# Kernel optimization log

Hardware: AMD Instinct MI355X
Metric: run time of the kernel (lower is better)

The kernel has to match this reference:

```python
import jax, jax.numpy as jnp
import numpy as np

NX, NY, NZ = 128, 128, 8
N_VOX = NX * NY * NZ
V, C, HF, WF = 6, 64, 116, 200
PAD_H, PAD_W = 928.0, 1600.0  # img_pad_shape (input image after padding)
IMG_H, IMG_W = 928.0, 1600.0  # img_shape used for the valid-flag bounds check


def _make_proj_mats():
    # Structured lidar2img matrices: pinhole intrinsics + 6 yaw-distributed cameras.
    K = np.array([[500.0, 0, 400, 0], [0, 500.0, 232, 0], [0, 0, 1, 0], [0, 0, 0, 1]], dtype=np.float64)
    A = np.array([[0.0, -1, 0], [0, 0, -1], [1, 0, 0]], dtype=np.float64)  # lidar(x fwd,y left,z up)->cam(z fwd)
    mats = []
    for j in range(V):
        yaw = 2.0 * np.pi * j / V
        c, s = np.cos(yaw), np.sin(yaw)
        Rz = np.array([[c, s, 0], [-s, c, 0], [0, 0, 1]])
        T = np.eye(4)
        T[:3, :3] = A @ Rz
        T[:3, 3] = np.array([0.0, -1.0, 0.0])
        mats.append(K @ T)
    return jnp.asarray(np.stack(mats), dtype=jnp.float32)


def setup_inputs() -> dict:
    key = jax.random.key(0)
    k1, k2 = jax.random.split(key)
    x_fov = jax.random.normal(k1, (1, V, C, HF, WF), dtype=jnp.float32)
    lo = jnp.array([-50.0, -50.0, -5.0], jnp.float32)
    span = jnp.array([100.0, 100.0, 8.0], jnp.float32)
    points = jax.random.uniform(k2, (N_VOX, 3), dtype=jnp.float32) * span + lo
    proj_mats = _make_proj_mats()
    return {"x_fov": x_fov, "points": points, "proj_mats": proj_mats}


def _bilinear_sample(feat, px, py):
    # feat [C,HF,WF]; px/py [N] in feature-map pixel coords.
    # Matches F.grid_sample(mode='bilinear', padding_mode='zeros', align_corners=False).
    x0 = jnp.floor(px)
    y0 = jnp.floor(py)
    wx1 = px - x0
    wy1 = py - y0

    def gather(xi, yi, w):
        inb = (xi >= 0) & (xi < WF) & (yi >= 0) & (yi < HF)
        xc = jnp.clip(xi, 0, WF - 1).astype(jnp.int32)
        yc = jnp.clip(yi, 0, HF - 1).astype(jnp.int32)
        return feat[:, yc, xc] * (w * inb)[None, :]  # [C,N]

    return (gather(x0, y0, (1 - wx1) * (1 - wy1))
            + gather(x0 + 1, y0, wx1 * (1 - wy1))
            + gather(x0, y0 + 1, (1 - wx1) * wy1)
            + gather(x0 + 1, y0 + 1, wx1 * wy1))


def _forward(x_fov, points, proj_mats):
    n = points.shape[0]
    # points_cam2img: homogeneous projection, perspective divide
    pts_h = jnp.concatenate([points, jnp.ones((n, 1), points.dtype)], axis=-1)  # [N,4]
    cam = jnp.einsum('vij,nj->vni', proj_mats, pts_h)  # [V,N,4]
    depth = cam[..., 2]
    d_safe = jnp.where(jnp.abs(depth) > 1e-6, depth, 1e-6)
    u = cam[..., 0] / d_safe  # image-plane x in input-image pixels (scale=1, crop=0, no flip)
    v = cam[..., 1] / d_safe
    # valid_flag: in front of camera and inside img_shape
    valid = (depth > 0) & (u > 0) & (u < IMG_W) & (v > 0) & (v < IMG_H)  # [V,N]
    # normalize by img_pad_shape then map to feature-map pixels (align_corners=False)
    px = u / PAD_W * WF - 0.5
    py = v / PAD_H * HF - 0.5
    feats = jax.vmap(_bilinear_sample)(x_fov[0], px, py)  # [V,C,N]
    feats = feats * valid[:, None, :].astype(feats.dtype)
    vol = feats.sum(0)  # [C,N] masked sum over views
    cnt = valid.sum(0).astype(feats.dtype)  # [N]
    vol = jnp.where(cnt > 0, vol, 0.0) / jnp.clip(cnt, 0.001)[None, :]
    # reshape(n_voxels[::-1] + [-1]).permute(3,2,1,0) -> [C,NX,NY,NZ]
    out = jnp.transpose(vol.reshape(C, NZ, NY, NX), (0, 3, 2, 1))
    return out[None]  # [1,C,NX,NY,NZ]


def reference(x_fov, points, proj_mats):
    return _forward(x_fov, points, proj_mats)
```

## Files before the change

### kernel.cpp

```cpp
#include <hip/hip_runtime.h>
#include <hip/hip_bf16.h>
#include <hip/hip_fp16.h>

#define NXv 128
#define NYv 128
#define NZv 8
#define NVOX (NXv * NYv * NZv)
#define NV 6
#define NC 64
#define HFv 116
#define WFv 200
#define PLANE (HFv * WFv)

#define FT_BYTES ((size_t)NV * PLANE * NC * 2)

__device__ inline unsigned int f2bf(float f) {
  unsigned int x = __float_as_uint(f);
  unsigned int r = x + 0x7fffu + ((x >> 16) & 1u);
  return (r >> 16) & 0xffffu;
}
__device__ inline float bf_lo(unsigned int q) { return __uint_as_float(q << 16); }
__device__ inline float bf_hi(unsigned int q) { return __uint_as_float(q & 0xffff0000u); }

__device__ inline unsigned short f2h_bits(float f) {
  __half h = __float2half(f);
  return *reinterpret_cast<unsigned short*>(&h);
}
__device__ inline float h_bits2f(unsigned short u) {
  __half_raw r; r.x = u;
  __half h = *reinterpret_cast<__half*>(&r);
  return __half2float(h);
}

__global__ __launch_bounds__(256) void transpose_feat_bf16(
    const float* __restrict__ in, unsigned int* __restrict__ out32) {
  __shared__ float tile[64][65];
  const int v  = blockIdx.y;
  const int p0 = blockIdx.x * 64;
  const float* src = in + (size_t)v * NC * PLANE;
  unsigned int* dst = out32 + (size_t)v * PLANE * (NC / 2);
  const int t = threadIdx.x;

#pragma unroll
  for (int i = 0; i < 4; ++i) {
    const int idx = i * 256 + t;
    const int c  = idx >> 4;
    const int p4 = idx & 15;
    const int pp = p0 + p4 * 4;
    if (pp < PLANE) {
      const float4 f = *(const float4*)(src + (size_t)c * PLANE + pp);
      tile[p4 * 4 + 0][c] = f.x;
      tile[p4 * 4 + 1][c] = f.y;
      tile[p4 * 4 + 2][c] = f.z;
      tile[p4 * 4 + 3][c] = f.w;
    }
  }
  __syncthreads();

#pragma unroll
  for (int i = 0; i < 2; ++i) {
    const int idx = i * 256 + t;
    const int p   = idx >> 3;
    const int c8  = idx & 7;
    const int pp  = p0 + p;
    if (pp < PLANE) {
      uint4 w;
      w.x = f2bf(tile[p][c8 * 8 + 0]) | (f2bf(tile[p][c8 * 8 + 1]) << 16);
      w.y = f2bf(tile[p][c8 * 8 + 2]) | (f2bf(tile[p][c8 * 8 + 3]) << 16);
      w.z = f2bf(tile[p][c8 * 8 + 4]) | (f2bf(tile[p][c8 * 8 + 5]) << 16);
      w.w = f2bf(tile[p][c8 * 8 + 6]) | (f2bf(tile[p][c8 * 8 + 7]) << 16);
      *(uint4*)(dst + (size_t)pp * 32 + c8 * 4) = w;
    }
  }
}

__global__ __launch_bounds__(256, 8) void gather_fused(
    const uint4* __restrict__ feat4,
    const float* __restrict__ points,
    const float* __restrict__ proj,
    float* __restrict__ out) {
  __shared__ unsigned short tile_h[64][66];
  __shared__ uint4 pdl[64 * NV];
  __shared__ int   cntl[64];
  __shared__ float invl[64];
  __shared__ float projl[96];

  const int bi   = blockIdx.x;
  const int xcd  = bi & 7;
  const int r    = bi >> 3;
  const int tid  = xcd * 2 + (r >> 7);
  const int q    = r & 127;
  const int ix   = (tid & 3) * 32 + (q & 31);
  const int iyg  = (tid >> 2) * 4 + (q >> 5);
  const int iy0g = iyg * 8;

  const int t    = threadIdx.x;
  const int lane = t & 63;
  const int wave = t >> 6;

  if (t < 96) projl[t] = proj[t];
  if (t < 64) cntl[t] = 0;
  __syncthreads();

  for (int task = t; task < 64 * NV; task += 256) {
    const int slot = task / NV;
    const int v    = task - slot * NV;
    const int j    = slot >> 3;
    const int iz   = slot & 7;
    const int n    = iz * (NXv * NYv) + (iy0g + j) * NXv + ix;

    const float x = points[n * 3 + 0];
    const float y = points[n * 3 + 1];
    const float z = points[n * 3 + 2];

    const float* M = projl + v * 16;
    const float cx = M[0] * x + M[1] * y + M[2]  * z + M[3];
    const float cy = M[4] * x + M[5] * y + M[6]  * z + M[7];
    const float cz = M[8] * x + M[9] * y + M[10] * z + M[11];

    const float dz = (fabsf(cz) > 1e-6f) ? cz : 1e-6f;
    const float u  = cx / dz;
    const float vv = cy / dz;

    const bool valid = (cz > 0.0f) && (u > 0.0f) && (u < 1600.0f) &&
                       (vv > 0.0f) && (vv < 928.0f);
    if (valid) {
      const float px = u  / 1600.0f * 200.0f - 0.5f;
      const float py = vv / 928.0f  * 116.0f - 0.5f;
      const float fx0 = floorf(px);
      const float fy0 = floorf(py);
      const float wx1 = px - fx0;
      const float wy1 = py - fy0;
      const float wx0 = 1.0f - wx1;
      const float wy0 = 1.0f - wy1;
      const int ix0 = (int)fx0;
      const int iy0 = (int)fy0;

      const bool bx0 = (ix0 >= 0) && (ix0 < WFv);
      const bool bx1 = (ix0 + 1 >= 0) && (ix0 + 1 < WFv);
      const bool by0 = (iy0 >= 0) && (iy0 < HFv);
      const bool by1 = (iy0 + 1 >= 0) && (iy0 + 1 < HFv);

      const int xc0 = min(max(ix0, 0), WFv - 1);
      const int xc1 = min(max(ix0 + 1, 0), WFv - 1);
      const int yc0 = min(max(iy0, 0), HFv - 1);
      const int yc1 = min(max(iy0 + 1, 0), HFv - 1);
      const unsigned int p00 = (unsigned int)(yc0 * WFv + xc0);
      const unsigned int p10 = (unsigned int)(yc0 * WFv + xc1);
      const unsigned int p01 = (unsigned int)(yc1 * WFv + xc0);
      const unsigned int p11 = (unsigned int)(yc1 * WFv + xc1);
      const unsigned int uv = (unsigned int)v;

      uint4 rec;
      rec.x = p00 | ((uv & 1u) << 15) | (p10 << 16) | (((uv >> 1) & 1u) << 31);
      rec.y = p01 | (((uv >> 2) & 1u) << 15) | (p11 << 16);
      rec.z = (unsigned int)f2h_bits((bx0 && by0) ? wx0 * wy0 : 0.0f) |
              ((unsigned int)f2h_bits((bx1 && by0) ? wx1 * wy0 : 0.0f) << 16);
      rec.w = (unsigned int)f2h_bits((bx0 && by1) ? wx0 * wy1 : 0.0f) |
              ((unsigned int)f2h_bits((bx1 && by1) ? wx1 * wy1 : 0.0f) << 16);
      const int idx = atomicAdd(&cntl[slot], 1);
      pdl[slot * NV + idx] = rec;
    }
  }
  __syncthreads();
  if (t < 64) { const int c = cntl[t]; invl[t] = (c > 0) ? 1.0f / (float)c : 0.0f; }
  __syncthreads();

  const int pg = lane >> 3;
  const int ch = lane & 7;

#pragma unroll
  for (int it = 0; it < 2; ++it) {
    const int sl = wave * 16 + it * 8 + pg;
    const int mycnt = cntl[sl];
    int km = mycnt;
    km = max(km, __shfl_xor(km, 8));
    km = max(km, __shfl_xor(km, 16));
    km = max(km, __shfl_xor(km, 32));

    float acc[8];
#pragma unroll
    for (int j2 = 0; j2 < 8; ++j2) acc[j2] = 0.0f;

    for (int k = 0; k < km; ++k) {
      if (k < mycnt) {
        const uint4 rec = pdl[sl * NV + k];
        const unsigned int p00 = rec.x & 0x7fffu;
        const unsigned int p10 = (rec.x >> 16) & 0x7fffu;
        const unsigned int p01 = rec.y & 0x7fffu;
        const unsigned int p11 = (rec.y >> 16) & 0x7fffu;
        const unsigned int v = ((rec.x >> 15) & 1u) | (((rec.x >> 31) & 1u) << 1) |
                               (((rec.y >> 15) & 1u) << 2);
        const float w0 = h_bits2f((unsigned short)(rec.z & 0xffffu));
        const float w1 = h_bits2f((unsigned short)(rec.z >> 16));
        const float w2 = h_bits2f((unsigned short)(rec.w & 0xffffu));
        const float w3 = h_bits2f((unsigned short)(rec.w >> 16));

        const uint4* fb = feat4 + (size_t)v * PLANE * 8 + ch;
        const uint4 q0 = fb[(size_t)p00 * 8];
        const uint4 q1 = fb[(size_t)p10 * 8];
        const uint4 q2 = fb[(size_t)p01 * 8];
        const uint4 q3 = fb[(size_t)p11 * 8];

        acc[0] = fmaf(w0, bf_lo(q0.x), acc[0]); acc[1] = fmaf(w0, bf_hi(q0.x), acc[1]);
        acc[2] = fmaf(w0, bf_lo(q0.y), acc[2]); acc[3] = fmaf(w0, bf_hi(q0.y), acc[3]);
        acc[4] = fmaf(w0, bf_lo(q0.z), acc[4]); acc[5] = fmaf(w0, bf_hi(q0.z), acc[5]);
        acc[6] = fmaf(w0, bf_lo(q0.w), acc[6]); acc[7] = fmaf(w0, bf_hi(q0.w), acc[7]);

        acc[0] = fmaf(w1, bf_lo(q1.x), acc[0]); acc[1] = fmaf(w1, bf_hi(q1.x), acc[1]);
        acc[2] = fmaf(w1, bf_lo(q1.y), acc[2]); acc[3] = fmaf(w1, bf_hi(q1.y), acc[3]);
        acc[4] = fmaf(w1, bf_lo(q1.z), acc[4]); acc[5] = fmaf(w1, bf_hi(q1.z), acc[5]);
        acc[6] = fmaf(w1, bf_lo(q1.w), acc[6]); acc[7] = fmaf(w1, bf_hi(q1.w), acc[7]);

        acc[0] = fmaf(w2, bf_lo(q2.x), acc[0]); acc[1] = fmaf(w2, bf_hi(q2.x), acc[1]);
        acc[2] = fmaf(w2, bf_lo(q2.y), acc[2]); acc[3] = fmaf(w2, bf_hi(q2.y), acc[3]);
        acc[4] = fmaf(w2, bf_lo(q2.z), acc[4]); acc[5] = fmaf(w2, bf_hi(q2.z), acc[5]);
        acc[6] = fmaf(w2, bf_lo(q2.w), acc[6]); acc[7] = fmaf(w2, bf_hi(q2.w), acc[7]);

        acc[0] = fmaf(w3, bf_lo(q3.x), acc[0]); acc[1] = fmaf(w3, bf_hi(q3.x), acc[1]);
        acc[2] = fmaf(w3, bf_lo(q3.y), acc[2]); acc[3] = fmaf(w3, bf_hi(q3.y), acc[3]);
        acc[4] = fmaf(w3, bf_lo(q3.z), acc[4]); acc[5] = fmaf(w3, bf_hi(q3.z), acc[5]);
        acc[6] = fmaf(w3, bf_lo(q3.w), acc[6]); acc[7] = fmaf(w3, bf_hi(q3.w), acc[7]);
      }
    }

    const float inv = invl[sl];
#pragma unroll
    for (int j2 = 0; j2 < 4; ++j2) {
      const unsigned int pk =
          (unsigned int)f2h_bits(acc[j2 * 2 + 0] * inv) |
          ((unsigned int)f2h_bits(acc[j2 * 2 + 1] * inv) << 16);
      *(unsigned int*)&tile_h[sl][ch * 8 + j2 * 2] = pk;
    }
  }

  __syncthreads();

  const size_t obase = (size_t)ix * (NYv * NZv) + (size_t)iy0g * NZv + lane;
#pragma unroll
  for (int i = 0; i < 16; ++i) {
    const int c = i * 4 + wave;
    const float val = h_bits2f(tile_h[lane][c]);
    __builtin_nontemporal_store(val, &out[(size_t)c * NVOX + obase]);
  }
}

__global__ __launch_bounds__(256) void sample_fallback(
    const float* __restrict__ feat,
    const float* __restrict__ points,
    const float* __restrict__ proj,
    float* __restrict__ out) {
  const int wave = threadIdx.x >> 6;
  const int lane = threadIdx.x & 63;
  const int n = blockIdx.x * 4 + wave;

  const float x = points[n * 3 + 0];
  const float y = points[n * 3 + 1];
  const float z = points[n * 3 + 2];

  float acc = 0.0f;
  int cnt = 0;

#pragma unroll
  for (int v = 0; v < NV; ++v) {
    const float* M = proj + v * 16;
    const float cx = M[0] * x + M[1] * y + M[2]  * z + M[3];
    const float cy = M[4] * x + M[5] * y + M[6]  * z + M[7];
    const float cz = M[8] * x + M[9] * y + M[10] * z + M[11];
    const float dz = (fabsf(cz) > 1e-6f) ? cz : 1e-6f;
    const float u  = cx / dz;
    const float vv = cy / dz;
    const bool valid = (cz > 0.0f) && (u > 0.0f) && (u < 1600.0f) &&
                       (vv > 0.0f) && (vv < 928.0f);
    if (!valid) continue;
    cnt++;
    const float px = u  / 1600.0f * 200.0f - 0.5f;
    const float py = vv / 928.0f  * 116.0f - 0.5f;
    const float fx0 = floorf(px);
    const float fy0 = floorf(py);
    const float wx1 = px - fx0;
    const float wy1 = py - fy0;
    const float wx0 = 1.0f - wx1;
    const float wy0 = 1.0f - wy1;
    const int ix0 = (int)fx0;
    const int iy0 = (int)fy0;
    const float w00 = wx0 * wy0, w10 = wx1 * wy0, w01 = wx0 * wy1, w11 = wx1 * wy1;
    const float* basev = feat + ((size_t)v * NC + lane) * PLANE;
    auto tap = [&](int xi, int yi, float w) {
      if (xi >= 0 && xi < WFv && yi >= 0 && yi < HFv)
        acc += w * basev[yi * WFv + xi];
    };
    tap(ix0,     iy0,     w00);
    tap(ix0 + 1, iy0,     w10);
    tap(ix0,     iy0 + 1, w01);
    tap(ix0 + 1, iy0 + 1, w11);
  }

  const float scale = (cnt > 0) ? (1.0f / (float)cnt) : 0.0f;
  const int iz  = n >> 14;
  const int rem = n & 16383;
  const int iy  = rem >> 7;
  const int ixx = rem & 127;
  out[(((size_t)lane * NXv + ixx) * NYv + iy) * NZv + iz] = acc * scale;
}

extern "C" void kernel_launch(void* const* d_in, const int* in_sizes, int n_in,
                              void* d_out, int out_size, void* d_ws, size_t ws_size,
                              hipStream_t stream) {
  const float* x_fov  = (const float*)d_in[0];
  const float* points = (const float*)d_in[1];
  const float* proj   = (const float*)d_in[2];
  float* out = (float*)d_out;

  if (ws_size >= FT_BYTES) {
    unsigned int* ft = (unsigned int*)d_ws;
    dim3 tgrid((PLANE + 63) / 64, NV);
    transpose_feat_bf16<<<tgrid, 256, 0, stream>>>(x_fov, ft);
    gather_fused<<<NXv * NYv / 8, 256, 0, stream>>>((const uint4*)ft, points, proj, out);
  } else {
    sample_fallback<<<NVOX / 4, 256, 0, stream>>>(x_fov, points, proj, out);
  }
}
```

Baseline: 99.87 us.

## Move point projection into the transpose kernel and stage records through workspace

The per-voxel projection and bilinear-record building now run in the first kernel, alongside a grid-strided bf16 transpose of the feature maps. The records, counts and inverse counts go to global workspace, and the gather kernel just loads them into shared memory. The aim is to overlap the projection math with the memory-bound transpose and take that latency off the gather kernel's critical path. In exchange it adds workspace traffic for the records, changes the prep grid to 2048 blocks at occupancy 4, and uses nontemporal loads for the input features.

```diff
diff --git a/kernel.cpp b/kernel.cpp
--- a/kernel.cpp
+++ b/kernel.cpp
@@ -11,8 +11,15 @@
 #define HFv 116
 #define WFv 200
 #define PLANE (HFv * WFv)
-
-#define FT_BYTES ((size_t)NV * PLANE * NC * 2)
+#define NBLK (NXv * NYv / 8)
+#define NTILE ((PLANE + 63) / 64 * NV)
+
+#define FT_BYTES  ((size_t)NV * PLANE * NC * 2)
+#define PD_BYTES  ((size_t)NBLK * 64 * NV * 16)
+#define CNT_BYTES ((size_t)NBLK * 64 * 4)
+#define INV_BYTES ((size_t)NBLK * 64 * 4)
+
+typedef float floatx4 __attribute__((ext_vector_type(4)));
 
 __device__ inline unsigned int f2bf(float f) {
   unsigned int x = __float_as_uint(f);
@@ -32,71 +39,31 @@
   return __half2float(h);
 }
 
-__global__ __launch_bounds__(256) void transpose_feat_bf16(
-    const float* __restrict__ in, unsigned int* __restrict__ out32) {
-  __shared__ float tile[64][65];
-  const int v  = blockIdx.y;
-  const int p0 = blockIdx.x * 64;
-  const float* src = in + (size_t)v * NC * PLANE;
-  unsigned int* dst = out32 + (size_t)v * PLANE * (NC / 2);
-  const int t = threadIdx.x;
-
-#pragma unroll
-  for (int i = 0; i < 4; ++i) {
-    const int idx = i * 256 + t;
-    const int c  = idx >> 4;
-    const int p4 = idx & 15;
-    const int pp = p0 + p4 * 4;
-    if (pp < PLANE) {
-      const float4 f = *(const float4*)(src + (size_t)c * PLANE + pp);
-      tile[p4 * 4 + 0][c] = f.x;
-      tile[p4 * 4 + 1][c] = f.y;
-      tile[p4 * 4 + 2][c] = f.z;
-      tile[p4 * 4 + 3][c] = f.w;
-    }
-  }
-  __syncthreads();
-
-#pragma unroll
-  for (int i = 0; i < 2; ++i) {
-    const int idx = i * 256 + t;
-    const int p   = idx >> 3;
-    const int c8  = idx & 7;
-    const int pp  = p0 + p;
-    if (pp < PLANE) {
-      uint4 w;
-      w.x = f2bf(tile[p][c8 * 8 + 0]) | (f2bf(tile[p][c8 * 8 + 1]) << 16);
-      w.y = f2bf(tile[p][c8 * 8 + 2]) | (f2bf(tile[p][c8 * 8 + 3]) << 16);
-      w.z = f2bf(tile[p][c8 * 8 + 4]) | (f2bf(tile[p][c8 * 8 + 5]) << 16);
-      w.w = f2bf(tile[p][c8 * 8 + 6]) | (f2bf(tile[p][c8 * 8 + 7]) << 16);
-      *(uint4*)(dst + (size_t)pp * 32 + c8 * 4) = w;
-    }
-  }
-}
-
-__global__ __launch_bounds__(256, 8) void gather_fused(
-    const uint4* __restrict__ feat4,
+__device__ inline void block_geom(int bi, int& ix, int& iy0g) {
+  const int xcd = bi & 7;
+  const int r   = bi >> 3;
+  const int tid = xcd * 2 + (r >> 7);
+  const int q   = r & 127;
+  ix   = (tid & 3) * 32 + (q & 31);
+  iy0g = ((tid >> 2) * 4 + (q >> 5)) * 8;
+}
+
+__global__ __launch_bounds__(256, 4) void prep_kernel(
+    const float* __restrict__ in,
+    unsigned int* __restrict__ feat_out,
     const float* __restrict__ points,
     const float* __restrict__ proj,
-    float* __restrict__ out) {
-  __shared__ unsigned short tile_h[64][66];
-  __shared__ uint4 pdl[64 * NV];
+    uint4* __restrict__ pdata,
+    unsigned int* __restrict__ cnt_out,
+    float* __restrict__ inv_out) {
+  __shared__ float tile[64][65];
   __shared__ int   cntl[64];
-  __shared__ float invl[64];
   __shared__ float projl[96];
 
-  const int bi   = blockIdx.x;
-  const int xcd  = bi & 7;
-  const int r    = bi >> 3;
-  const int tid  = xcd * 2 + (r >> 7);
-  const int q    = r & 127;
-  const int ix   = (tid & 3) * 32 + (q & 31);
-  const int iyg  = (tid >> 2) * 4 + (q >> 5);
-  const int iy0g = iyg * 8;
-
-  const int t    = threadIdx.x;
-  const int lane = t & 63;
-  const int wave = t >> 6;
+  const int b = blockIdx.x;
+  const int t = threadIdx.x;
+  int ix, iy0g;
+  block_geom(b, ix, iy0g);
 
   if (t < 96) projl[t] = proj[t];
   if (t < 64) cntl[t] = 0;
@@ -159,11 +126,84 @@
       rec.w = (unsigned int)f2h_bits((bx0 && by1) ? wx0 * wy1 : 0.0f) |
               ((unsigned int)f2h_bits((bx1 && by1) ? wx1 * wy1 : 0.0f) << 16);
       const int idx = atomicAdd(&cntl[slot], 1);
-      pdl[slot * NV + idx] = rec;
+      pdata[(size_t)b * (64 * NV) + slot * NV + idx] = rec;
     }
   }
   __syncthreads();
-  if (t < 64) { const int c = cntl[t]; invl[t] = (c > 0) ? 1.0f / (float)c : 0.0f; }
+  if (t < 64) {
+    const int c = cntl[t];
+    cnt_out[(size_t)b * 64 + t] = (unsigned int)c;
+    inv_out[(size_t)b * 64 + t] = (c > 0) ? 1.0f / (float)c : 0.0f;
+  }
+
+  for (int tl = b; tl < NTILE; tl += NBLK) {
+    const int v  = tl / 363;
+    const int p0 = (tl - v * 363) * 64;
+    const float* src = in + (size_t)v * NC * PLANE;
+    unsigned int* dst = feat_out + (size_t)v * PLANE * (NC / 2);
+
+    __syncthreads();
+#pragma unroll
+    for (int i = 0; i < 4; ++i) {
+      const int idx = i * 256 + t;
+      const int c  = idx >> 4;
+      const int p4 = idx & 15;
+      const int pp = p0 + p4 * 4;
+      if (pp < PLANE) {
+        const floatx4 f = __builtin_nontemporal_load(
+            (const floatx4*)(src + (size_t)c * PLANE + pp));
+        tile[p4 * 4 + 0][c] = f.x;
+        tile[p4 * 4 + 1][c] = f.y;
+        tile[p4 * 4 + 2][c] = f.z;
+        tile[p4 * 4 + 3][c] = f.w;
+      }
+    }
+    __syncthreads();
+#pragma unroll
+    for (int i = 0; i < 2; ++i) {
+      const int idx = i * 256 + t;
+      const int p   = idx >> 3;
+      const int c8  = idx & 7;
+      const int pp  = p0 + p;
+      if (pp < PLANE) {
+        uint4 w;
+        w.x = f2bf(tile[p][c8 * 8 + 0]) | (f2bf(tile[p][c8 * 8 + 1]) << 16);
+        w.y = f2bf(tile[p][c8 * 8 + 2]) | (f2bf(tile[p][c8 * 8 + 3]) << 16);
+        w.z = f2bf(tile[p][c8 * 8 + 4]) | (f2bf(tile[p][c8 * 8 + 5]) << 16);
+        w.w = f2bf(tile[p][c8 * 8 + 6]) | (f2bf(tile[p][c8 * 8 + 7]) << 16);
+        *(uint4*)(dst + (size_t)pp * 32 + c8 * 4) = w;
+      }
+    }
+  }
+}
+
+__global__ __launch_bounds__(256, 8) void gather_kernel(
+    const uint4* __restrict__ feat4,
+    const uint4* __restrict__ pdata,
+    const unsigned int* __restrict__ cntg,
+    const float* __restrict__ invg,
+    float* __restrict__ out) {
+  __shared__ unsigned short tile_h[64][66];
+  __shared__ uint4 pdl[64 * NV];
+  __shared__ int   cntl[64];
+  __shared__ float invl[64];
+
+  const int b = blockIdx.x;
+  const int t = threadIdx.x;
+  int ix, iy0g;
+  block_geom(b, ix, iy0g);
+
+  const int lane = t & 63;
+  const int wave = t >> 6;
+
+  {
+    const uint4* src = pdata + (size_t)b * (64 * NV);
+    for (int i = t; i < 64 * NV; i += 256) pdl[i] = src[i];
+    if (t < 64) {
+      cntl[t] = (int)cntg[(size_t)b * 64 + t];
+      invl[t] = invg[(size_t)b * 64 + t];
+    }
+  }
   __syncthreads();
 
   const int pg = lane >> 3;
@@ -312,11 +352,15 @@
   const float* proj   = (const float*)d_in[2];
   float* out = (float*)d_out;
 
-  if (ws_size >= FT_BYTES) {
+  const size_t need = FT_BYTES + PD_BYTES + CNT_BYTES + INV_BYTES;
+  if (ws_size >= need) {
     unsigned int* ft = (unsigned int*)d_ws;
-    dim3 tgrid((PLANE + 63) / 64, NV);
-    transpose_feat_bf16<<<tgrid, 256, 0, stream>>>(x_fov, ft);
-    gather_fused<<<NXv * NYv / 8, 256, 0, stream>>>((const uint4*)ft, points, proj, out);
+    uint4* pd = (uint4*)((char*)d_ws + FT_BYTES);
+    unsigned int* cg = (unsigned int*)((char*)d_ws + FT_BYTES + PD_BYTES);
+    float* ig = (float*)((char*)d_ws + FT_BYTES + PD_BYTES + CNT_BYTES);
+
+    prep_kernel<<<NBLK, 256, 0, stream>>>(x_fov, ft, points, proj, pd, cg, ig);
+    gather_kernel<<<NBLK, 256, 0, stream>>>((const uint4*)ft, pd, cg, ig, out);
   } else {
     sample_fallback<<<NVOX / 4, 256, 0, stream>>>(x_fov, points, proj, out);
   }
```

Measured after the change: 106.8 us. 1.07x slower.
